# Optimization experiments

Measured on AMD Instinct MI355X. Metric: run time of the kernel, lower is better.

The kernel has to match this reference:

```python
import jax, jax.numpy as jnp
import numpy as np

D_MODEL, D_FF, N_EXPERTS, TOP_K = 1024, 4096, 8, 2
B, S = 2, 2048


def setup_inputs() -> dict:
    key = jax.random.key(0)
    ks = jax.random.split(key, 7)
    scale = 0.02
    return {
        "x": jax.random.normal(ks[0], (B, S, D_MODEL), dtype=jnp.float32),
        "W1": jax.random.normal(ks[1], (N_EXPERTS, D_MODEL, D_FF), dtype=jnp.float32) * scale,
        "b1": jnp.zeros((N_EXPERTS, D_FF), dtype=jnp.float32),
        "W2": jax.random.normal(ks[2], (N_EXPERTS, D_FF, D_MODEL), dtype=jnp.float32) * scale,
        "b2": jnp.zeros((N_EXPERTS, D_MODEL), dtype=jnp.float32),
        "Wg": jax.random.normal(ks[3], (D_MODEL, N_EXPERTS), dtype=jnp.float32) * scale,
        "bg": jnp.zeros((N_EXPERTS,), dtype=jnp.float32),
    }


def reference(x, W1, b1, W2, b2, Wg, bg):
    # x: [B, S, d_model]
    Bx, Sx, d = x.shape
    E = W1.shape[0]
    # Gate + top-k routing (softmax over the top-k scores, as in the torch code)
    logits = jnp.einsum("bsd,de->bse", x, Wg) + bg            # [B,S,E]
    topk_scores, topk_idx = jax.lax.top_k(logits, TOP_K)       # [B,S,K]
    topk_scores = jax.nn.softmax(topk_scores, axis=-1)

    tokens = x.reshape(-1, d)                                  # [T,d]
    idx_flat = topk_idx.reshape(-1, TOP_K)                     # [T,K]
    sc_flat = topk_scores.reshape(-1, TOP_K)                   # [T,K]
    # Per-token combine weight for each expert: sum_k score_k * 1[idx_k == e]
    comb = (jax.nn.one_hot(idx_flat, E, dtype=x.dtype) * sc_flat[..., None]).sum(axis=1)  # [T,E]

    # Dense grouped expert MLP (zero combine weight kills non-selected experts)
    h = jnp.einsum("td,edf->etf", tokens, W1) + b1[:, None, :]  # [E,T,d_ff]
    even = (jnp.arange(E) % 2 == 0)[:, None, None]
    # torch nn.GELU default = exact (erf); odd experts use SiLU
    a = jnp.where(even, jax.nn.gelu(h, approximate=False), jax.nn.silu(h))
    y = jnp.einsum("etf,efd->etd", a, W2) + b2[:, None, :]      # [E,T,d_model]
    out = jnp.einsum("te,etd->td", comb, y)                     # [T,d_model]
    # Dropout is identity in eval mode
    return out.reshape(Bx, Sx, d)
```

## Files before the change

### kernel.cpp

```cpp
#include <hip/hip_runtime.h>
#include <stdint.h>

#define T_TOK 4096
#define DM 1024
#define DF 4096
#define NE 8

typedef __attribute__((ext_vector_type(8))) short bf16x8;
typedef __attribute__((ext_vector_type(4))) float f32x4;

__device__ __forceinline__ float b2f(unsigned short u) {
    union { unsigned int i; float f; } v; v.i = ((unsigned int)u) << 16; return v.f;
}
__device__ __forceinline__ unsigned short f2b(float f) {
    unsigned int i = __float_as_uint(f);
    unsigned int r = (i + 0x7FFFu + ((i >> 16) & 1u)) >> 16;
    return (unsigned short)r;
}
__device__ __forceinline__ void load_lds16(const void* g, void* l) {
    __builtin_amdgcn_global_load_lds((__attribute__((address_space(1))) void*)(g),
                                     (__attribute__((address_space(3))) void*)(l), 16, 0, 0);
}

__device__ __forceinline__ float fexp2(float x) {
#if __has_builtin(__builtin_amdgcn_exp2f)
    return __builtin_amdgcn_exp2f(x);
#else
    return exp2f(x);
#endif
}
__device__ __forceinline__ float frcp(float x) {
#if __has_builtin(__builtin_amdgcn_rcpf)
    return __builtin_amdgcn_rcpf(x);
#else
    return 1.0f / x;
#endif
}

__device__ __forceinline__ float gelu_f(float h) {
    float z = h * 0.70710678118654752f;
    float az = fabsf(z);
    float t = frcp(1.0f + 0.3275911f * az);
    float p = ((((1.061405429f * t - 1.453152027f) * t + 1.421413741f) * t
                - 0.284496736f) * t + 0.254829592f) * t;
    float e = fexp2(-1.4426950408889634f * az * az);
    float er = 1.0f - p * e;
    er = (z < 0.f) ? -er : er;
    return 0.5f * h * (1.0f + er);
}
__device__ __forceinline__ float silu_f(float h) {
    return h * frcp(1.0f + fexp2(-1.4426950408889634f * h));
}

__global__ __launch_bounds__(256) void detect_kernel(const unsigned short* __restrict__ xu,
                                                     int* __restrict__ flag) {
    const int i = (blockIdx.x * 256 + threadIdx.x) * 4;
    uint2 v = *(const uint2*)&xu[i];
    unsigned int a = v.x, b = v.y;
    int found = 0;
    if (((a >> 7)  & 0xFF) == 0xFF) found = 1;
    if (((a >> 23) & 0xFF) == 0xFF) found = 1;
    if (((b >> 7)  & 0xFF) == 0xFF) found = 1;
    if (((b >> 23) & 0xFF) == 0xFF) found = 1;
    if (__ballot(found) != 0 && (threadIdx.x & 63) == 0) atomicOr(flag, 1);
}

__global__ __launch_bounds__(256) void convx_kernel(const void* __restrict__ xin,
                                                    const int* __restrict__ flag,
                                                    unsigned short* __restrict__ xb) {
    const size_t i = ((size_t)blockIdx.x * 256 + threadIdx.x) * 8;
    if (*flag) {
        const float* xf = (const float*)xin + i;
        float4 a = *(const float4*)xf;
        float4 b = *(const float4*)(xf + 4);
        alignas(16) unsigned short t[8] = { f2b(a.x), f2b(a.y), f2b(a.z), f2b(a.w),
                                            f2b(b.x), f2b(b.y), f2b(b.z), f2b(b.w) };
        *(uint4*)(xb + i) = *(const uint4*)t;
    } else {
        *(uint4*)(xb + i) = *(const uint4*)((const unsigned short*)xin + i);
    }
}

__global__ void convf_kernel(const void* __restrict__ src, const int* __restrict__ flag,
                             float* __restrict__ dst, int n) {
    int i = blockIdx.x * 256 + threadIdx.x;
    if (i < n) dst[i] = (*flag) ? ((const float*)src)[i] : b2f(((const unsigned short*)src)[i]);
}

__global__ __launch_bounds__(256) void transpose_kernel(const void* __restrict__ in,
                                                        unsigned short* __restrict__ out,
                                                        int R, int C, const int* __restrict__ flag) {
    __shared__ unsigned short tile[64][65];
    const int isf = *flag;
    const size_t base = (size_t)blockIdx.z * R * C;
    const int r0 = blockIdx.y * 64, c0 = blockIdx.x * 64;
    const int lr = threadIdx.x >> 2;
    const int lc = (threadIdx.x & 3) * 16;
    if (isf) {
        const float* src = (const float*)in + base + (size_t)(r0 + lr) * C + c0 + lc;
#pragma unroll
        for (int q = 0; q < 4; q++) {
            float4 v = *(const float4*)(src + q * 4);
            tile[lr][lc + q * 4 + 0] = f2b(v.x);
            tile[lr][lc + q * 4 + 1] = f2b(v.y);
            tile[lr][lc + q * 4 + 2] = f2b(v.z);
            tile[lr][lc + q * 4 + 3] = f2b(v.w);
        }
    } else {
        const unsigned short* src = (const unsigned short*)in + base + (size_t)(r0 + lr) * C + c0 + lc;
#pragma unroll
        for (int q = 0; q < 2; q++) {
            uint4 v = *(const uint4*)(src + q * 8);
            unsigned int w[4] = { v.x, v.y, v.z, v.w };
#pragma unroll
            for (int j = 0; j < 4; j++) {
                tile[lr][lc + q * 8 + 2 * j]     = (unsigned short)(w[j] & 0xffff);
                tile[lr][lc + q * 8 + 2 * j + 1] = (unsigned short)(w[j] >> 16);
            }
        }
    }
    __syncthreads();
    const int oc = threadIdx.x >> 2;
    const int oj = (threadIdx.x & 3) * 16;
    alignas(16) unsigned short tmp[16];
#pragma unroll
    for (int j = 0; j < 16; j++) tmp[j] = tile[oj + j][oc];
    unsigned short* dst = out + base + (size_t)(c0 + oc) * R + r0 + oj;
    *(uint4*)(dst) = *(const uint4*)(tmp);
    *(uint4*)(dst + 8) = *(const uint4*)(tmp + 8);
}

__global__ __launch_bounds__(256) void gate_kernel(
    const void* __restrict__ x, const void* __restrict__ Wg, const void* __restrict__ bg,
    const int* __restrict__ flag, int* __restrict__ cnt,
    int* __restrict__ tok_e, float* __restrict__ tok_s) {
    const int isf = *flag;
    const int wave = threadIdx.x >> 6, lane = threadIdx.x & 63;
    const int t = blockIdx.x * 4 + wave;
    float p[8] = {0.f,0.f,0.f,0.f,0.f,0.f,0.f,0.f};
    if (isf) {
        const float* xr = (const float*)x + (size_t)t * DM;
        const float* wg = (const float*)Wg;
        for (int i = lane; i < DM; i += 64) {
            float xv = xr[i];
            float4 a = *(const float4*)(wg + (size_t)i * 8);
            float4 b = *(const float4*)(wg + (size_t)i * 8 + 4);
            p[0] += xv * a.x; p[1] += xv * a.y; p[2] += xv * a.z; p[3] += xv * a.w;
            p[4] += xv * b.x; p[5] += xv * b.y; p[6] += xv * b.z; p[7] += xv * b.w;
        }
    } else {
        const unsigned short* xr = (const unsigned short*)x + (size_t)t * DM;
        const unsigned short* wg = (const unsigned short*)Wg;
        for (int i = lane; i < DM; i += 64) {
            float xv = b2f(xr[i]);
            uint4 wv = *(const uint4*)(wg + (size_t)i * 8);
            p[0] += xv * b2f((unsigned short)(wv.x & 0xffff));
            p[1] += xv * b2f((unsigned short)(wv.x >> 16));
            p[2] += xv * b2f((unsigned short)(wv.y & 0xffff));
            p[3] += xv * b2f((unsigned short)(wv.y >> 16));
            p[4] += xv * b2f((unsigned short)(wv.z & 0xffff));
            p[5] += xv * b2f((unsigned short)(wv.z >> 16));
            p[6] += xv * b2f((unsigned short)(wv.w & 0xffff));
            p[7] += xv * b2f((unsigned short)(wv.w >> 16));
        }
    }
    for (int off = 32; off > 0; off >>= 1)
        for (int e = 0; e < 8; e++) p[e] += __shfl_down(p[e], off);
    if (lane == 0) {
        for (int e = 0; e < 8; e++)
            p[e] += isf ? ((const float*)bg)[e] : b2f(((const unsigned short*)bg)[e]);
        int e0 = 0;
        for (int e = 1; e < 8; e++) if (p[e] > p[e0]) e0 = e;
        int e1 = (e0 == 0) ? 1 : 0;
        for (int e = 0; e < 8; e++) if (e != e0 && p[e] > p[e1]) e1 = e;
        float z = expf(p[e1] - p[e0]);
        float s0 = 1.f / (1.f + z);
        tok_e[2 * t] = e0; tok_e[2 * t + 1] = e1;
        tok_s[2 * t] = s0; tok_s[2 * t + 1] = z * s0;
        atomicAdd(&cnt[e0], 1); atomicAdd(&cnt[e1], 1);
    }
}

__global__ void scan_kernel(const int* __restrict__ cnt, int* __restrict__ offs) {
    if (threadIdx.x == 0) {
        int s = 0;
        for (int e = 0; e < NE; e++) { offs[e] = s; s += cnt[e]; }
    }
}

__global__ __launch_bounds__(256) void place_kernel(
    const int* __restrict__ tok_e, const int* __restrict__ offs, int* __restrict__ cnt2,
    int* __restrict__ tok_list, int* __restrict__ slot_of) {
    const int t = blockIdx.x * 256 + threadIdx.x;
    for (int k = 0; k < 2; k++) {
        int e = tok_e[2 * t + k];
        int slot = atomicAdd(&cnt2[e], 1);
        int idx = offs[e] + slot;
        tok_list[idx] = t;
        slot_of[2 * t + k] = idx;
    }
}

__global__ __launch_bounds__(256) void gemm1_kernel(
    const unsigned short* __restrict__ xb, const unsigned short* __restrict__ W1T,
    const float* __restrict__ b1f, const int* __restrict__ tok_list,
    const int* __restrict__ offs, const int* __restrict__ cnt,
    unsigned short* __restrict__ act) {
    const int e = blockIdx.z, by = blockIdx.y, bx = blockIdx.x;
    const int ne = cnt[e];
    if (by * 128 >= ne) return;
    const int off_e = offs[e];
    __shared__ unsigned short Asm[2][128 * 32];
    __shared__ unsigned short Bsm[2][128 * 32];
    __shared__ int toks[128];
    const int tid = threadIdx.x, w = tid >> 6, lane = tid & 63;
    if (tid < 128) {
        int r = by * 128 + tid;
        toks[tid] = tok_list[off_e + (r < ne ? r : ne - 1)];
    }
    __syncthreads();
    const int arow0 = w * 16 + (lane >> 2);
    const int s_sw = (lane >> 3) & 3;
    const int acol = (((lane & 3) ^ s_sw) * 8);
    const int tok0 = toks[arow0], tok1 = toks[arow0 + 64];
    const unsigned short* gA0 = xb + (size_t)tok0 * DM + acol;
    const unsigned short* gA1 = xb + (size_t)tok1 * DM + acol;
    const unsigned short* Wte = W1T + (size_t)e * DF * DM;
    const unsigned short* gB0 = Wte + (size_t)(bx * 128 + arow0) * DM + acol;
    const unsigned short* gB1 = gB0 + (size_t)64 * DM;
    f32x4 acc[4][4] = {};
    const int mb = (w >> 1) * 64, nb = (w & 1) * 64;
    const int rdoff = (((lane >> 4) ^ ((lane >> 1) & 3)) * 8);

#define STAGE1(buf, kk) do { \
        load_lds16(gA0 + (kk), &Asm[buf][(w) * 16 * 32]); \
        load_lds16(gA1 + (kk), &Asm[buf][(w + 4) * 16 * 32]); \
        load_lds16(gB0 + (kk), &Bsm[buf][(w) * 16 * 32]); \
        load_lds16(gB1 + (kk), &Bsm[buf][(w + 4) * 16 * 32]); \
    } while (0)

    STAGE1(0, 0);
    __syncthreads();
    int cur = 0;
    for (int kk = 0; kk < DM; kk += 32) {
        if (kk + 32 < DM) STAGE1(cur ^ 1, kk + 32);
        bf16x8 af[4], bfv[4];
#pragma unroll
        for (int i = 0; i < 4; i++)
            af[i] = *(const bf16x8*)&Asm[cur][(mb + i * 16 + (lane & 15)) * 32 + rdoff];
#pragma unroll
        for (int j = 0; j < 4; j++)
            bfv[j] = *(const bf16x8*)&Bsm[cur][(nb + j * 16 + (lane & 15)) * 32 + rdoff];
        __builtin_amdgcn_s_setprio(1);
#pragma unroll
        for (int i = 0; i < 4; i++)
#pragma unroll
            for (int j = 0; j < 4; j++)
                acc[i][j] = __builtin_amdgcn_mfma_f32_16x16x32_bf16(af[i], bfv[j], acc[i][j], 0, 0, 0);
        __builtin_amdgcn_s_setprio(0);
        __syncthreads();
        cur ^= 1;
    }
#undef STAGE1

    const bool even_e = (e & 1) == 0;
    const float* b1e = b1f + (size_t)e * DF + bx * 128;
#pragma unroll
    for (int i = 0; i < 4; i++) {
#pragma unroll
        for (int r = 0; r < 4; r++) {
            int m = mb + i * 16 + ((lane >> 4) * 4) + r;
            int grow = by * 128 + m;
            if (grow < ne) {
                unsigned short* dst = act + (size_t)(off_e + grow) * DF + bx * 128;
#pragma unroll
                for (int j = 0; j < 4; j++) {
                    int n = nb + j * 16 + (lane & 15);
                    float h = acc[i][j][r] + b1e[n];
                    float a = even_e ? gelu_f(h) : silu_f(h);
                    dst[n] = f2b(a);
                }
            }
        }
    }
}

__global__ __launch_bounds__(256) void gemm2_kernel(
    const unsigned short* __restrict__ act, const unsigned short* __restrict__ W2T,
    const float* __restrict__ b2f, const int* __restrict__ offs,
    const int* __restrict__ cnt, float* __restrict__ yall) {
    const int e = blockIdx.z, by = blockIdx.y, bx = blockIdx.x;
    const int ne = cnt[e];
    if (by * 128 >= ne) return;
    const int off_e = offs[e];
    __shared__ unsigned short Asm[2][128 * 32];
    __shared__ unsigned short Bsm[2][128 * 32];
    const int tid = threadIdx.x, w = tid >> 6, lane = tid & 63;
    const int arow0 = w * 16 + (lane >> 2);
    const int s_sw = (lane >> 3) & 3;
    const int acol = (((lane & 3) ^ s_sw) * 8);
    int r0 = by * 128 + arow0;       if (r0 > ne - 1) r0 = ne - 1;
    int r1 = by * 128 + arow0 + 64;  if (r1 > ne - 1) r1 = ne - 1;
    const unsigned short* gA0 = act + (size_t)(off_e + r0) * DF + acol;
    const unsigned short* gA1 = act + (size_t)(off_e + r1) * DF + acol;
    const unsigned short* Wte = W2T + (size_t)e * DM * DF;
    const unsigned short* gB0 = Wte + (size_t)(bx * 128 + arow0) * DF + acol;
    const unsigned short* gB1 = gB0 + (size_t)64 * DF;
    f32x4 acc[4][4] = {};
    const int mb = (w >> 1) * 64, nb = (w & 1) * 64;
    const int rdoff = (((lane >> 4) ^ ((lane >> 1) & 3)) * 8);

#define STAGE2(buf, kk) do { \
        load_lds16(gA0 + (kk), &Asm[buf][(w) * 16 * 32]); \
        load_lds16(gA1 + (kk), &Asm[buf][(w + 4) * 16 * 32]); \
        load_lds16(gB0 + (kk), &Bsm[buf][(w) * 16 * 32]); \
        load_lds16(gB1 + (kk), &Bsm[buf][(w + 4) * 16 * 32]); \
    } while (0)

    STAGE2(0, 0);
    __syncthreads();
    int cur = 0;
    for (int kk = 0; kk < DF; kk += 32) {
        if (kk + 32 < DF) STAGE2(cur ^ 1, kk + 32);
        bf16x8 af[4], bfv[4];
#pragma unroll
        for (int i = 0; i < 4; i++)
            af[i] = *(const bf16x8*)&Asm[cur][(mb + i * 16 + (lane & 15)) * 32 + rdoff];
#pragma unroll
        for (int j = 0; j < 4; j++)
            bfv[j] = *(const bf16x8*)&Bsm[cur][(nb + j * 16 + (lane & 15)) * 32 + rdoff];
        __builtin_amdgcn_s_setprio(1);
#pragma unroll
        for (int i = 0; i < 4; i++)
#pragma unroll
            for (int j = 0; j < 4; j++)
                acc[i][j] = __builtin_amdgcn_mfma_f32_16x16x32_bf16(af[i], bfv[j], acc[i][j], 0, 0, 0);
        __builtin_amdgcn_s_setprio(0);
        __syncthreads();
        cur ^= 1;
    }
#undef STAGE2

    const float* b2e = b2f + (size_t)e * DM + bx * 128;
#pragma unroll
    for (int i = 0; i < 4; i++) {
#pragma unroll
        for (int r = 0; r < 4; r++) {
            int m = mb + i * 16 + ((lane >> 4) * 4) + r;
            int grow = by * 128 + m;
            if (grow < ne) {
                float* dst = yall + (size_t)(off_e + grow) * DM + bx * 128;
#pragma unroll
                for (int j = 0; j < 4; j++) {
                    int n = nb + j * 16 + (lane & 15);
                    dst[n] = acc[i][j][r] + b2e[n];
                }
            }
        }
    }
}

__global__ __launch_bounds__(256) void combine_kernel(
    const float* __restrict__ yall, const int* __restrict__ slot_of,
    const float* __restrict__ tok_s, void* __restrict__ out, const int* __restrict__ flag) {
    const int t = blockIdx.x;
    const int c = threadIdx.x * 4;
    const int s0i = slot_of[2 * t], s1i = slot_of[2 * t + 1];
    const float w0 = tok_s[2 * t], w1 = tok_s[2 * t + 1];
    float4 a = *(const float4*)&yall[(size_t)s0i * DM + c];
    float4 b = *(const float4*)&yall[(size_t)s1i * DM + c];
    float4 r;
    r.x = w0 * a.x + w1 * b.x;
    r.y = w0 * a.y + w1 * b.y;
    r.z = w0 * a.z + w1 * b.z;
    r.w = w0 * a.w + w1 * b.w;
    if (*flag) {
        *(float4*)((float*)out + (size_t)t * DM + c) = r;
    } else {
        ushort4 o;
        o.x = f2b(r.x); o.y = f2b(r.y); o.z = f2b(r.z); o.w = f2b(r.w);
        *(ushort4*)((unsigned short*)out + (size_t)t * DM + c) = o;
    }
}

extern "C" void kernel_launch(void* const* d_in, const int* in_sizes, int n_in,
                              void* d_out, int out_size, void* d_ws, size_t ws_size,
                              hipStream_t stream) {
    (void)in_sizes; (void)n_in; (void)out_size; (void)ws_size;
    const void* x  = d_in[0];
    const void* W1 = d_in[1];
    const void* b1 = d_in[2];
    const void* W2 = d_in[3];
    const void* b2 = d_in[4];
    const void* Wg = d_in[5];
    const void* bg = d_in[6];

    uint8_t* wsb = (uint8_t*)d_ws;
    int* ip = (int*)wsb;
    int* flag  = ip;
    int* cnt   = ip + 8;
    int* cnt2  = ip + 16;
    int* offs  = ip + 24;
    int* tok_e = ip + 32;
    float* tok_s  = (float*)(tok_e + 2 * T_TOK);
    int* tok_list = (int*)(tok_s + 2 * T_TOK);
    int* slot_of  = tok_list + 2 * T_TOK;
    size_t head = (size_t)((uint8_t*)(slot_of + 2 * T_TOK) - wsb);
    head = (head + 255) & ~(size_t)255;
    float* b1f = (float*)(wsb + head);
    float* b2f = b1f + (size_t)NE * DF;
    unsigned short* xb  = (unsigned short*)(b2f + (size_t)NE * DM);
    unsigned short* W1T = xb + (size_t)T_TOK * DM;
    unsigned short* W2T = W1T + (size_t)NE * DM * DF;
    unsigned short* actb = W2T + (size_t)NE * DM * DF;
    float* yall = (float*)W1T;

    hipMemsetAsync(ip, 0, 128, stream);
    detect_kernel<<<256, 256, 0, stream>>>((const unsigned short*)x, flag);
    convx_kernel<<<(T_TOK * DM) / 2048, 256, 0, stream>>>(x, flag, xb);
    convf_kernel<<<(NE * DF) / 256, 256, 0, stream>>>(b1, flag, b1f, NE * DF);
    convf_kernel<<<(NE * DM) / 256, 256, 0, stream>>>(b2, flag, b2f, NE * DM);
    transpose_kernel<<<dim3(DF / 64, DM / 64, NE), 256, 0, stream>>>(W1, W1T, DM, DF, flag);
    transpose_kernel<<<dim3(DM / 64, DF / 64, NE), 256, 0, stream>>>(W2, W2T, DF, DM, flag);
    gate_kernel<<<T_TOK / 4, 256, 0, stream>>>(x, Wg, bg, flag, cnt, tok_e, tok_s);
    scan_kernel<<<1, 64, 0, stream>>>(cnt, offs);
    place_kernel<<<T_TOK / 256, 256, 0, stream>>>(tok_e, offs, cnt2, tok_list, slot_of);
    gemm1_kernel<<<dim3(DF / 128, T_TOK / 128, NE), 256, 0, stream>>>(xb, W1T, b1f, tok_list, offs, cnt, actb);
    gemm2_kernel<<<dim3(DM / 128, T_TOK / 128, NE), 256, 0, stream>>>(actb, W2T, b2f, offs, cnt, yall);
    combine_kernel<<<T_TOK, 256, 0, stream>>>(yall, slot_of, tok_s, d_out, flag);
}
```

Measured before the change: 746.0 us.

## Split-K gemm2 across two halves, merge prep kernels, deterministic compaction

The second expert GEMM now splits its K dimension in two, doubling the grid so more blocks run when the M extent per expert is small. The halves are written to separate buffers and summed in the combine kernel. The bias conversion and both weight transposes are each merged into a single launch. The atomic gate count, scan and place kernels become one ballot-based compaction kernel. This cuts launch count and raises gemm2 occupancy, at the cost of extra partial-sum traffic and a compaction that runs on only 8 blocks.

```diff
diff --git a/kernel.cpp b/kernel.cpp
--- a/kernel.cpp
+++ b/kernel.cpp
@@ -81,19 +81,38 @@
     }
 }
 
-__global__ void convf_kernel(const void* __restrict__ src, const int* __restrict__ flag,
-                             float* __restrict__ dst, int n) {
-    int i = blockIdx.x * 256 + threadIdx.x;
-    if (i < n) dst[i] = (*flag) ? ((const float*)src)[i] : b2f(((const unsigned short*)src)[i]);
-}
-
-__global__ __launch_bounds__(256) void transpose_kernel(const void* __restrict__ in,
-                                                        unsigned short* __restrict__ out,
-                                                        int R, int C, const int* __restrict__ flag) {
+__global__ void convf_kernel(const void* __restrict__ b1, const void* __restrict__ b2,
+                             const int* __restrict__ flag,
+                             float* __restrict__ d1, float* __restrict__ d2) {
+    const int i = blockIdx.x * 256 + threadIdx.x;
+    const int isf = *flag;
+    if (i < NE * DF) {
+        d1[i] = isf ? ((const float*)b1)[i] : b2f(((const unsigned short*)b1)[i]);
+    } else {
+        int j = i - NE * DF;
+        d2[j] = isf ? ((const float*)b2)[j] : b2f(((const unsigned short*)b2)[j]);
+    }
+}
+
+__global__ __launch_bounds__(256) void transpose_kernel(
+    const void* __restrict__ in1, const void* __restrict__ in2,
+    unsigned short* __restrict__ out1, unsigned short* __restrict__ out2,
+    const int* __restrict__ flag) {
     __shared__ unsigned short tile[64][65];
     const int isf = *flag;
-    const size_t base = (size_t)blockIdx.z * R * C;
-    const int r0 = blockIdx.y * 64, c0 = blockIdx.x * 64;
+    const void* in; unsigned short* out;
+    int R, C, rt, ct; size_t base;
+    if (blockIdx.z < 8) {
+        in = in1; out = out1; R = DM; C = DF;
+        base = (size_t)blockIdx.z * R * C;
+        rt = blockIdx.y; ct = blockIdx.x;
+    } else {
+        in = in2; out = out2; R = DF; C = DM;
+        base = (size_t)(blockIdx.z - 8) * R * C;
+        ct = blockIdx.x & 15;
+        rt = (blockIdx.y << 2) | (blockIdx.x >> 4);
+    }
+    const int r0 = rt * 64, c0 = ct * 64;
     const int lr = threadIdx.x >> 2;
     const int lc = (threadIdx.x & 3) * 16;
     if (isf) {
@@ -132,7 +151,7 @@
 
 __global__ __launch_bounds__(256) void gate_kernel(
     const void* __restrict__ x, const void* __restrict__ Wg, const void* __restrict__ bg,
-    const int* __restrict__ flag, int* __restrict__ cnt,
+    const int* __restrict__ flag,
     int* __restrict__ tok_e, float* __restrict__ tok_s) {
     const int isf = *flag;
     const int wave = threadIdx.x >> 6, lane = threadIdx.x & 63;
@@ -177,27 +196,67 @@
         float s0 = 1.f / (1.f + z);
         tok_e[2 * t] = e0; tok_e[2 * t + 1] = e1;
         tok_s[2 * t] = s0; tok_s[2 * t + 1] = z * s0;
-        atomicAdd(&cnt[e0], 1); atomicAdd(&cnt[e1], 1);
-    }
-}
-
-__global__ void scan_kernel(const int* __restrict__ cnt, int* __restrict__ offs) {
-    if (threadIdx.x == 0) {
-        int s = 0;
-        for (int e = 0; e < NE; e++) { offs[e] = s; s += cnt[e]; }
-    }
-}
-
-__global__ __launch_bounds__(256) void place_kernel(
-    const int* __restrict__ tok_e, const int* __restrict__ offs, int* __restrict__ cnt2,
-    int* __restrict__ tok_list, int* __restrict__ slot_of) {
-    const int t = blockIdx.x * 256 + threadIdx.x;
-    for (int k = 0; k < 2; k++) {
-        int e = tok_e[2 * t + k];
-        int slot = atomicAdd(&cnt2[e], 1);
-        int idx = offs[e] + slot;
-        tok_list[idx] = t;
-        slot_of[2 * t + k] = idx;
+    }
+}
+
+__global__ __launch_bounds__(256) void compact_kernel(const int* __restrict__ tok_e,
+                                                      int* __restrict__ cnt,
+                                                      int* __restrict__ offs,
+                                                      int* __restrict__ tok_list,
+                                                      int* __restrict__ slot_of) {
+    const int e = blockIdx.x;
+    const int tid = threadIdx.x, w = tid >> 6, lane = tid & 63;
+    int c[8] = {0,0,0,0,0,0,0,0};
+    for (int i = tid; i < 2 * T_TOK; i += 256) {
+        int v = tok_e[i];
+#pragma unroll
+        for (int q = 0; q < 8; q++) c[q] += (v == q);
+    }
+    for (int off = 32; off > 0; off >>= 1)
+#pragma unroll
+        for (int q = 0; q < 8; q++) c[q] += __shfl_down(c[q], off);
+    __shared__ int ws4[4][8];
+    if (lane == 0)
+#pragma unroll
+        for (int q = 0; q < 8; q++) ws4[w][q] = c[q];
+    __syncthreads();
+    __shared__ int base_s;
+    __shared__ int wtot[4];
+    __shared__ int running;
+    if (tid == 0) {
+        int s = 0, be = 0, ce = 0;
+        for (int q = 0; q < 8; q++) {
+            int t = ws4[0][q] + ws4[1][q] + ws4[2][q] + ws4[3][q];
+            if (q == e) { be = s; ce = t; }
+            s += t;
+        }
+        base_s = be;
+        cnt[e] = ce;
+        offs[e] = be;
+        running = 0;
+    }
+    __syncthreads();
+    const int base = base_s;
+    for (int i0 = 0; i0 < 2 * T_TOK; i0 += 256) {
+        const int i = i0 + tid;
+        const int v = tok_e[i];
+        const bool pred = (v == e);
+        unsigned long long m = __ballot(pred);
+        int rank = __popcll(m & ((1ull << lane) - 1ull));
+        if (lane == 0) wtot[w] = __popcll(m);
+        __syncthreads();
+        int woff = 0;
+        for (int ww = 0; ww < w; ww++) woff += wtot[ww];
+        const int tot = wtot[0] + wtot[1] + wtot[2] + wtot[3];
+        const int r = running;
+        if (pred) {
+            int pos = base + r + woff + rank;
+            tok_list[pos] = i >> 1;
+            slot_of[i] = pos;
+        }
+        __syncthreads();
+        if (tid == 0) running += tot;
+        __syncthreads();
     }
 }
 
@@ -287,9 +346,10 @@
 
 __global__ __launch_bounds__(256) void gemm2_kernel(
     const unsigned short* __restrict__ act, const unsigned short* __restrict__ W2T,
-    const float* __restrict__ b2f, const int* __restrict__ offs,
-    const int* __restrict__ cnt, float* __restrict__ yall) {
-    const int e = blockIdx.z, by = blockIdx.y, bx = blockIdx.x;
+    const float* __restrict__ b2fp, const int* __restrict__ offs,
+    const int* __restrict__ cnt, float* __restrict__ yall0, float* __restrict__ yall1) {
+    const int e = blockIdx.z & 7, h = blockIdx.z >> 3;
+    const int by = blockIdx.y, bx = blockIdx.x;
     const int ne = cnt[e];
     if (by * 128 >= ne) return;
     const int off_e = offs[e];
@@ -299,12 +359,13 @@
     const int arow0 = w * 16 + (lane >> 2);
     const int s_sw = (lane >> 3) & 3;
     const int acol = (((lane & 3) ^ s_sw) * 8);
+    const int kbase = h * (DF / 2);
     int r0 = by * 128 + arow0;       if (r0 > ne - 1) r0 = ne - 1;
     int r1 = by * 128 + arow0 + 64;  if (r1 > ne - 1) r1 = ne - 1;
-    const unsigned short* gA0 = act + (size_t)(off_e + r0) * DF + acol;
-    const unsigned short* gA1 = act + (size_t)(off_e + r1) * DF + acol;
+    const unsigned short* gA0 = act + (size_t)(off_e + r0) * DF + kbase + acol;
+    const unsigned short* gA1 = act + (size_t)(off_e + r1) * DF + kbase + acol;
     const unsigned short* Wte = W2T + (size_t)e * DM * DF;
-    const unsigned short* gB0 = Wte + (size_t)(bx * 128 + arow0) * DF + acol;
+    const unsigned short* gB0 = Wte + (size_t)(bx * 128 + arow0) * DF + kbase + acol;
     const unsigned short* gB1 = gB0 + (size_t)64 * DF;
     f32x4 acc[4][4] = {};
     const int mb = (w >> 1) * 64, nb = (w & 1) * 64;
@@ -320,8 +381,8 @@
     STAGE2(0, 0);
     __syncthreads();
     int cur = 0;
-    for (int kk = 0; kk < DF; kk += 32) {
-        if (kk + 32 < DF) STAGE2(cur ^ 1, kk + 32);
+    for (int kk = 0; kk < DF / 2; kk += 32) {
+        if (kk + 32 < DF / 2) STAGE2(cur ^ 1, kk + 32);
         bf16x8 af[4], bfv[4];
 #pragma unroll
         for (int i = 0; i < 4; i++)
@@ -341,7 +402,8 @@
     }
 #undef STAGE2
 
-    const float* b2e = b2f + (size_t)e * DM + bx * 128;
+    float* yall = h ? yall1 : yall0;
+    const float* b2e = b2fp + (size_t)e * DM + bx * 128;
 #pragma unroll
     for (int i = 0; i < 4; i++) {
 #pragma unroll
@@ -353,7 +415,7 @@
 #pragma unroll
                 for (int j = 0; j < 4; j++) {
                     int n = nb + j * 16 + (lane & 15);
-                    dst[n] = acc[i][j][r] + b2e[n];
+                    dst[n] = acc[i][j][r] + (h ? 0.0f : b2e[n]);
                 }
             }
         }
@@ -361,19 +423,22 @@
 }
 
 __global__ __launch_bounds__(256) void combine_kernel(
-    const float* __restrict__ yall, const int* __restrict__ slot_of,
-    const float* __restrict__ tok_s, void* __restrict__ out, const int* __restrict__ flag) {
+    const float* __restrict__ yall0, const float* __restrict__ yall1,
+    const int* __restrict__ slot_of, const float* __restrict__ tok_s,
+    void* __restrict__ out, const int* __restrict__ flag) {
     const int t = blockIdx.x;
     const int c = threadIdx.x * 4;
     const int s0i = slot_of[2 * t], s1i = slot_of[2 * t + 1];
     const float w0 = tok_s[2 * t], w1 = tok_s[2 * t + 1];
-    float4 a = *(const float4*)&yall[(size_t)s0i * DM + c];
-    float4 b = *(const float4*)&yall[(size_t)s1i * DM + c];
+    float4 a0 = *(const float4*)&yall0[(size_t)s0i * DM + c];
+    float4 a1 = *(const float4*)&yall1[(size_t)s0i * DM + c];
+    float4 b0 = *(const float4*)&yall0[(size_t)s1i * DM + c];
+    float4 b1 = *(const float4*)&yall1[(size_t)s1i * DM + c];
     float4 r;
-    r.x = w0 * a.x + w1 * b.x;
-    r.y = w0 * a.y + w1 * b.y;
-    r.z = w0 * a.z + w1 * b.z;
-    r.w = w0 * a.w + w1 * b.w;
+    r.x = w0 * (a0.x + a1.x) + w1 * (b0.x + b1.x);
+    r.y = w0 * (a0.y + a1.y) + w1 * (b0.y + b1.y);
+    r.z = w0 * (a0.z + a1.z) + w1 * (b0.z + b1.z);
+    r.w = w0 * (a0.w + a1.w) + w1 * (b0.w + b1.w);
     if (*flag) {
         *(float4*)((float*)out + (size_t)t * DM + c) = r;
     } else {
@@ -413,19 +478,18 @@
     unsigned short* W1T = xb + (size_t)T_TOK * DM;
     unsigned short* W2T = W1T + (size_t)NE * DM * DF;
     unsigned short* actb = W2T + (size_t)NE * DM * DF;
-    float* yall = (float*)W1T;
+    float* yall0 = (float*)W1T;
+    float* yall1 = yall0 + (size_t)2 * T_TOK * DM;
+    (void)cnt2;
 
     hipMemsetAsync(ip, 0, 128, stream);
     detect_kernel<<<256, 256, 0, stream>>>((const unsigned short*)x, flag);
     convx_kernel<<<(T_TOK * DM) / 2048, 256, 0, stream>>>(x, flag, xb);
-    convf_kernel<<<(NE * DF) / 256, 256, 0, stream>>>(b1, flag, b1f, NE * DF);
-    convf_kernel<<<(NE * DM) / 256, 256, 0, stream>>>(b2, flag, b2f, NE * DM);
-    transpose_kernel<<<dim3(DF / 64, DM / 64, NE), 256, 0, stream>>>(W1, W1T, DM, DF, flag);
-    transpose_kernel<<<dim3(DM / 64, DF / 64, NE), 256, 0, stream>>>(W2, W2T, DF, DM, flag);
-    gate_kernel<<<T_TOK / 4, 256, 0, stream>>>(x, Wg, bg, flag, cnt, tok_e, tok_s);
-    scan_kernel<<<1, 64, 0, stream>>>(cnt, offs);
-    place_kernel<<<T_TOK / 256, 256, 0, stream>>>(tok_e, offs, cnt2, tok_list, slot_of);
+    convf_kernel<<<(NE * (DF + DM)) / 256, 256, 0, stream>>>(b1, b2, flag, b1f, b2f);
+    transpose_kernel<<<dim3(64, 16, 16), 256, 0, stream>>>(W1, W2, W1T, W2T, flag);
+    gate_kernel<<<T_TOK / 4, 256, 0, stream>>>(x, Wg, bg, flag, tok_e, tok_s);
+    compact_kernel<<<NE, 256, 0, stream>>>(tok_e, cnt, offs, tok_list, slot_of);
     gemm1_kernel<<<dim3(DF / 128, T_TOK / 128, NE), 256, 0, stream>>>(xb, W1T, b1f, tok_list, offs, cnt, actb);
-    gemm2_kernel<<<dim3(DM / 128, T_TOK / 128, NE), 256, 0, stream>>>(actb, W2T, b2f, offs, cnt, yall);
-    combine_kernel<<<T_TOK, 256, 0, stream>>>(yall, slot_of, tok_s, d_out, flag);
-}
+    gemm2_kernel<<<dim3(DM / 128, T_TOK / 128, NE * 2), 256, 0, stream>>>(actb, W2T, b2f, offs, cnt, yall0, yall1);
+    combine_kernel<<<T_TOK, 256, 0, stream>>>(yall0, yall1, slot_of, tok_s, d_out, flag);
+}
```

Measured after the change: 635.2 us. -14.9%, faster.
